# Performance work log

Hardware: AMD Instinct MI355X
Metric: run time of the kernel (lower is better)

## Reference

```python
import jax, jax.numpy as jnp
import numpy as np

B, N, E = 2, 50000, 400000
FIN, HID, OUT = 128, 128, 128
EPS = 1e-5  # BatchNorm1d default eps


def setup_inputs() -> dict:
    key = jax.random.key(0)
    ks = jax.random.split(key, 12)
    x = jax.random.normal(ks[0], (B, N, FIN), dtype=jnp.float32)
    row = jax.random.randint(ks[1], (E,), 0, N, dtype=jnp.int32)          # scatter dst
    col = jnp.concatenate([jnp.arange(N, dtype=jnp.int32),                # ensure deg>=1
                           jax.random.randint(ks[2], (E - N,), 0, N, dtype=jnp.int32)])
    edge_index = jnp.stack([row, col])                                    # [2, E]
    deg = jnp.zeros((N,), jnp.float32).at[col].add(1.0)                   # degree(col, N)
    dis = deg ** -0.5
    norm = (dis[row] * dis[col])[None, :, None]                           # [1, E, 1]
    W1 = jax.random.normal(ks[3], (HID, FIN), jnp.float32) / np.sqrt(FIN)
    b1 = jax.random.normal(ks[4], (HID,), jnp.float32) * 0.01
    g1 = jnp.ones((N,), jnp.float32)
    be1 = jnp.zeros((N,), jnp.float32)
    W2 = jax.random.normal(ks[5], (OUT, HID), jnp.float32) / np.sqrt(HID)
    b2 = jax.random.normal(ks[6], (OUT,), jnp.float32) * 0.01
    g2 = jnp.ones((N,), jnp.float32)
    be2 = jnp.zeros((N,), jnp.float32)
    return {"x": x, "edge_index": edge_index, "norm": norm,
            "W1": W1, "b1": b1, "g1": g1, "be1": be1,
            "W2": W2, "b2": b2, "g2": g2, "be2": be2}


def _gcn_layer(x, edge_index, norm, W, b, g, be):
    # Linear (dropout p=0 -> identity)
    h = jnp.einsum('bnf,of->bno', x, W) + b                 # [B, N, C]
    # BatchNorm1d(num_features=N): per-node stats over (batch, channel)
    mu = jnp.mean(h, axis=(0, 2), keepdims=True)            # [1, N, 1]
    var = jnp.var(h, axis=(0, 2), keepdims=True)            # biased, as torch
    y = g[None, :, None] * (h - mu) * jax.lax.rsqrt(var + EPS) + be[None, :, None]
    a = jax.nn.gelu(y, approximate=False)                   # torch GELU = exact erf
    # message passing: gather src nodes, scale by norm, scatter-add to dst
    msgs = a[:, edge_index[1], :] * norm                    # [B, E, C]
    return jnp.zeros_like(a).at[:, edge_index[0], :].add(msgs)


def reference(x, edge_index, norm, W1, b1, g1, be1, W2, b2, g2, be2):
    x = _gcn_layer(x, edge_index, norm, W1, b1, g1, be1)
    x = _gcn_layer(x, edge_index, norm, W2, b2, g2, be2)
    return x
```

## Files before the change

kernel.cpp:

```cpp
#include <hip/hip_runtime.h>
#include <math.h>

#define CC 128

typedef unsigned short u16;
typedef short bf16x8 __attribute__((ext_vector_type(8)));
typedef float f32x4 __attribute__((ext_vector_type(4)));

typedef __attribute__((address_space(3))) void lds_t;
typedef const __attribute__((address_space(1))) void gbl_t;

__device__ __forceinline__ u16 f2bf(float f) {
    union { float f; unsigned u; } v; v.f = f;
    unsigned u = v.u;
    return (u16)((u + 0x7FFFu + ((u >> 16) & 1u)) >> 16);
}
__device__ __forceinline__ float bf2f(unsigned hi16) {
    union { unsigned u; float f; } v; v.u = hi16 << 16; return v.f;
}
__device__ __forceinline__ unsigned cvt_pk(float lo, float hi) {
    unsigned r;
    asm("v_cvt_pk_bf16_f32 %0, %1, %2" : "=v"(r) : "v"(lo), "v"(hi));
    return r;
}

__device__ __forceinline__ float gelu_f(float y) {
    float xa = fabsf(y) * 0.70710678118654752f;
    float t  = __builtin_amdgcn_rcpf(fmaf(0.3275911f, xa, 1.0f));
    float p  = fmaf(1.061405429f, t, -1.453152027f);
    p = fmaf(p, t, 1.421413741f);
    p = fmaf(p, t, -0.284496736f);
    p = fmaf(p, t, 0.254829592f);
    p *= t;
    float e  = __expf(-xa * xa);
    float er = fmaf(-p, e, 1.0f);
    float s  = copysignf(er, y);
    return 0.5f * y * (1.0f + s);
}


__global__ __launch_bounds__(256) void k_zero_i32(int* __restrict__ p, int n) {
    int i = blockIdx.x * 256 + threadIdx.x;
    if (i < n) p[i] = 0;
}

__global__ __launch_bounds__(256) void k_hist(const int* __restrict__ row, int* __restrict__ cnt, int E) {
    int e = blockIdx.x * 256 + threadIdx.x;
    if (e < E) atomicAdd(&cnt[row[e]], 1);
}

__device__ __forceinline__ int wave_incl_scan(int v) {
    #pragma unroll
    for (int d = 1; d < 64; d <<= 1) {
        int t = __shfl_up(v, d);
        if ((threadIdx.x & 63) >= d) v += t;
    }
    return v;
}

__global__ __launch_bounds__(256) void k_scan_a(const int* __restrict__ cnt, int* __restrict__ bsum, int N) {
    int base = blockIdx.x * 1024 + threadIdx.x * 4;
    int s = 0;
    #pragma unroll
    for (int u = 0; u < 4; ++u) { int i = base + u; if (i < N) s += cnt[i]; }
    #pragma unroll
    for (int d = 32; d > 0; d >>= 1) s += __shfl_down(s, d);
    __shared__ int wsum[4];
    if ((threadIdx.x & 63) == 0) wsum[threadIdx.x >> 6] = s;
    __syncthreads();
    if (threadIdx.x == 0) bsum[blockIdx.x] = wsum[0] + wsum[1] + wsum[2] + wsum[3];
}

__global__ __launch_bounds__(64) void k_scan_b(const int* __restrict__ bsum, int* __restrict__ boff,
                                               int* __restrict__ off, int N, int nb) {
    int carry = 0;
    for (int base = 0; base < nb; base += 64) {
        int t = base + (int)threadIdx.x;
        int v = (t < nb) ? bsum[t] : 0;
        int incl = wave_incl_scan(v);
        if (t < nb) boff[t] = carry + incl - v;
        carry += __shfl(incl, 63);
    }
    if (threadIdx.x == 0) off[N] = carry;
}

__global__ __launch_bounds__(256) void k_scan_c(int* __restrict__ cnt, const int* __restrict__ boff,
                                                int* __restrict__ off, int N) {
    int t = threadIdx.x;
    int base = blockIdx.x * 1024 + t * 4;
    int v[4]; int s = 0;
    #pragma unroll
    for (int u = 0; u < 4; ++u) { int i = base + u; v[u] = (i < N) ? cnt[i] : 0; s += v[u]; }
    int incl = wave_incl_scan(s);
    __shared__ int wsum[4];
    int w = t >> 6, lane = t & 63;
    if (lane == 63) wsum[w] = incl;
    __syncthreads();
    int run = incl - s + boff[blockIdx.x];
    for (int ww = 0; ww < w; ++ww) run += wsum[ww];
    #pragma unroll
    for (int u = 0; u < 4; ++u) {
        int i = base + u;
        if (i < N) { off[i] = run; cnt[i] = 0; }
        run += v[u];
    }
}

__global__ __launch_bounds__(256) void k_fill(const int* __restrict__ row, const int* __restrict__ col,
                                              const float* __restrict__ nrm, const int* __restrict__ off,
                                              int* __restrict__ cur, int2* __restrict__ eg, int E) {
    int e = blockIdx.x * 256 + threadIdx.x;
    if (e < E) {
        int r = row[e];
        int p = off[r] + atomicAdd(&cur[r], 1);
        eg[p] = make_int2(col[e], __float_as_int(nrm[e]));
    }
}

__global__ __launch_bounds__(256) void k_wrepack(const float* __restrict__ W1, u16* __restrict__ Wp1,
                                                 const float* __restrict__ W2, u16* __restrict__ Wp2) {
    int i = blockIdx.x * 256 + threadIdx.x;
    if (i < 2 * CC * CC) {
        int is2 = (i >= CC * CC);
        int ii = is2 ? i - CC * CC : i;
        int j = ii & 7, l = (ii >> 3) & 63, s = (ii >> 9) & 3, t = ii >> 11;
        int r = 16 * t + (l & 15);
        int p = s * 32 + ((l >> 4) & 3) * 8 + j;
        if (is2) {
            int k = (p & 7) * 16 + (p >> 3);
            Wp2[ii] = f2bf(W2[r * CC + k]);
        } else {
            Wp1[ii] = f2bf(W1[r * CC + p]);
        }
    }
}

__global__ __launch_bounds__(256) void k_fused_l1(
    const float* __restrict__ X, const u16* __restrict__ Wp1, const u16* __restrict__ Wp2,
    const float* __restrict__ bias, const float* __restrict__ gamma, const float* __restrict__ beta,
    u16* __restrict__ Z, int N)
{
    __shared__ __align__(16) u16 WS[CC * CC];
    __shared__ __align__(16) unsigned TT[4][16][68];

    const int tid = threadIdx.x;
    const int w = tid >> 6;
    const int l = tid & 63;
    const int g = l >> 4;
    const int c = l & 15;
    const int n8 = blockIdx.x * 32 + w * 8;
    const bool valid = n8 < N;
    const int nbase = valid ? n8 : 0;

    #pragma unroll
    for (int it = 0; it < 8; ++it) {
        const u16* gsrc = Wp1 + it * 2048 + w * 512 + l * 8;
        u16* ldst = &WS[it * 2048 + w * 512];
        __builtin_amdgcn_global_load_lds((gbl_t*)gsrc, (lds_t*)ldst, 16, 0, 0);
    }

    const int ab = c >> 3;
    const int an = nbase + (c & 7);
    const float* xbase = X + ((size_t)ab * N + an) * CC + g * 8;
    bf16x8 af[4];
    #pragma unroll
    for (int s = 0; s < 4; ++s) {
        float4 lo = *(const float4*)(xbase + s * 32);
        float4 hi = *(const float4*)(xbase + s * 32 + 4);
        unsigned aw[4];
        aw[0] = cvt_pk(lo.x, lo.y); aw[1] = cvt_pk(lo.z, lo.w);
        aw[2] = cvt_pk(hi.x, hi.y); aw[3] = cvt_pk(hi.z, hi.w);
        af[s] = *(bf16x8*)aw;
    }

    float bb[8];
    #pragma unroll
    for (int t = 0; t < 8; ++t) bb[t] = bias[t * 16 + c];
    float gam[4], bet[4];
    #pragma unroll
    for (int r = 0; r < 4; ++r) {
        int p = (4 * g + r) & 7;
        gam[r] = gamma[nbase + p];
        bet[r] = beta[nbase + p];
    }

    __syncthreads();

    f32x4 acc[8];
    #pragma unroll
    for (int t = 0; t < 8; ++t) acc[t] = (f32x4){0.f, 0.f, 0.f, 0.f};
    #pragma unroll
    for (int s = 0; s < 4; ++s) {
        bf16x8 bf[8];
        #pragma unroll
        for (int t = 0; t < 8; ++t)
            bf[t] = *(const bf16x8*)&WS[((t * 4 + s) * 64 + l) * 8];
        #pragma unroll
        for (int t = 0; t < 8; ++t)
            acc[t] = __builtin_amdgcn_mfma_f32_16x16x32_bf16(af[s], bf[t], acc[t], 0, 0, 0);
    }

    __syncthreads();

    #pragma unroll
    for (int it = 0; it < 8; ++it) {
        const u16* gsrc = Wp2 + it * 2048 + w * 512 + l * 8;
        u16* ldst = &WS[it * 2048 + w * 512];
        __builtin_amdgcn_global_load_lds((gbl_t*)gsrc, (lds_t*)ldst, 16, 0, 0);
    }

    float rs[4] = {0.f, 0.f, 0.f, 0.f}, rq[4] = {0.f, 0.f, 0.f, 0.f};
    #pragma unroll
    for (int t = 0; t < 8; ++t)
        #pragma unroll
        for (int r = 0; r < 4; ++r) {
            float h = acc[t][r] + bb[t];
            acc[t][r] = h;
            rs[r] += h;
            rq[r] += h * h;
        }
    #pragma unroll
    for (int d = 1; d < 16; d <<= 1) {
        #pragma unroll
        for (int r = 0; r < 4; ++r) {
            rs[r] += __shfl_xor(rs[r], d);
            rq[r] += __shfl_xor(rq[r], d);
        }
    }
    #pragma unroll
    for (int r = 0; r < 4; ++r) {
        rs[r] += __shfl_xor(rs[r], 32);
        rq[r] += __shfl_xor(rq[r], 32);
    }

    #pragma unroll
    for (int r = 0; r < 4; ++r) {
        float mean = rs[r] * (1.f / 256.f);
        float var  = rq[r] * (1.f / 256.f) - mean * mean;
        float sc = gam[r] * rsqrtf(fmaxf(var, 0.f) + 1e-5f);
        float sh = bet[r] - mean * sc;
        #pragma unroll
        for (int t = 0; t < 8; ++t)
            acc[t][r] = gelu_f(acc[t][r] * sc + sh);
    }

    #pragma unroll
    for (int r = 0; r < 4; ++r) {
        unsigned tw[4];
        #pragma unroll
        for (int tt = 0; tt < 4; ++tt)
            tw[tt] = cvt_pk(acc[2 * tt][r], acc[2 * tt + 1][r]);
        *(uint4*)&TT[w][4 * g + r][c * 4] = *(uint4*)tw;
    }
    bf16x8 af2[4];
    #pragma unroll
    for (int s = 0; s < 4; ++s)
        af2[s] = *(const bf16x8*)&TT[w][c][s * 16 + g * 4];

    __syncthreads();

    f32x4 acc2[8];
    #pragma unroll
    for (int t = 0; t < 8; ++t) acc2[t] = (f32x4){0.f, 0.f, 0.f, 0.f};
    #pragma unroll
    for (int s = 0; s < 4; ++s) {
        bf16x8 bf[8];
        #pragma unroll
        for (int t = 0; t < 8; ++t)
            bf[t] = *(const bf16x8*)&WS[((t * 4 + s) * 64 + l) * 8];
        #pragma unroll
        for (int t = 0; t < 8; ++t)
            acc2[t] = __builtin_amdgcn_mfma_f32_16x16x32_bf16(af2[s], bf[t], acc2[t], 0, 0, 0);
    }

    if (valid) {
        #pragma unroll
        for (int r = 0; r < 4; ++r) {
            int rr = 4 * g + r;
            int db = rr >> 3, dn = n8 + (rr & 7);
            unsigned zw[4];
            #pragma unroll
            for (int tt = 0; tt < 4; ++tt)
                zw[tt] = cvt_pk(acc2[2 * tt][r], acc2[2 * tt + 1][r]);
            *(uint4*)(Z + ((size_t)dn * 2 + db) * CC + c * 8) = *(uint4*)zw;
        }
    }
}

__global__ __launch_bounds__(256) void k_agg_bn(
    const u16* __restrict__ Zin, const int* __restrict__ off, const int2* __restrict__ eg,
    const float* __restrict__ b2, const float* __restrict__ g2, const float* __restrict__ be2,
    u16* __restrict__ A2, int N)
{
    __shared__ u16 TW[4][256];
    int wv = threadIdx.x >> 6;
    int n = blockIdx.x * 4 + wv;
    if (n >= N) return;
    int l = threadIdx.x & 63;
    int p = l >> 5;
    int b = (l >> 4) & 1;
    int c = l & 15;
    const u16* Ab = Zin + b * CC + c * 8;
    int s = off[n], e = off[n + 1];
    float a[8] = {0.f, 0.f, 0.f, 0.f, 0.f, 0.f, 0.f, 0.f};
    for (int j = s; j < e; j += 8) {
        int i0 = j + p, i1 = j + 2 + p, i2 = j + 4 + p, i3 = j + 6 + p;
        int2 e0 = (i0 < e) ? eg[i0] : make_int2(0, 0);
        int2 e1 = (i1 < e) ? eg[i1] : make_int2(0, 0);
        int2 e2 = (i2 < e) ? eg[i2] : make_int2(0, 0);
        int2 e3 = (i3 < e) ? eg[i3] : make_int2(0, 0);
        bf16x8 v0 = *(const bf16x8*)(Ab + (size_t)e0.x * 256);
        bf16x8 v1 = *(const bf16x8*)(Ab + (size_t)e1.x * 256);
        bf16x8 v2 = *(const bf16x8*)(Ab + (size_t)e2.x * 256);
        bf16x8 v3 = *(const bf16x8*)(Ab + (size_t)e3.x * 256);
        float w0 = __int_as_float(e0.y), w1 = __int_as_float(e1.y);
        float w2 = __int_as_float(e2.y), w3 = __int_as_float(e3.y);
        #pragma unroll
        for (int q = 0; q < 8; ++q) {
            a[q] = fmaf(w0, bf2f((u16)v0[q]), a[q]);
            a[q] = fmaf(w1, bf2f((u16)v1[q]), a[q]);
            a[q] = fmaf(w2, bf2f((u16)v2[q]), a[q]);
            a[q] = fmaf(w3, bf2f((u16)v3[q]), a[q]);
        }
    }
    #pragma unroll
    for (int q = 0; q < 8; ++q) a[q] += __shfl_xor(a[q], 32);

    float ss = 0.f, qq = 0.f;
    #pragma unroll
    for (int t = 0; t < 8; ++t) {
        float h = a[t] + b2[t * 16 + c];
        a[t] = h;
        ss += h;
        qq += h * h;
    }
    #pragma unroll
    for (int d = 1; d < 32; d <<= 1) {
        ss += __shfl_xor(ss, d);
        qq += __shfl_xor(qq, d);
    }
    float mean = ss * (1.f / 256.f);
    float var  = qq * (1.f / 256.f) - mean * mean;
    float sc = g2[n] * rsqrtf(fmaxf(var, 0.f) + 1e-5f);
    float sh = be2[n] - mean * sc;

    if (l < 32) {
        #pragma unroll
        for (int t = 0; t < 8; ++t)
            TW[wv][b * CC + t * 16 + c] = f2bf(gelu_f(a[t] * sc + sh));
    }
    if (l < 32) {
        bf16x8 v = *(const bf16x8*)&TW[wv][l * 8];
        *(bf16x8*)(A2 + (size_t)n * 256 + l * 8) = v;
    }
}

__global__ __launch_bounds__(256) void k_agg_out(
    const u16* __restrict__ A2, const int* __restrict__ off, const int2* __restrict__ eg,
    float* __restrict__ Out, int N)
{
    int n = blockIdx.x * 4 + (threadIdx.x >> 6);
    if (n >= N) return;
    int l = threadIdx.x & 63;
    int p = l >> 5;
    int sl = l & 31;
    const u16* Ab = A2 + sl * 8;
    int s = off[n], e = off[n + 1];
    float a[8] = {0.f, 0.f, 0.f, 0.f, 0.f, 0.f, 0.f, 0.f};
    for (int j = s; j < e; j += 8) {
        int i0 = j + p, i1 = j + 2 + p, i2 = j + 4 + p, i3 = j + 6 + p;
        int2 e0 = (i0 < e) ? eg[i0] : make_int2(0, 0);
        int2 e1 = (i1 < e) ? eg[i1] : make_int2(0, 0);
        int2 e2 = (i2 < e) ? eg[i2] : make_int2(0, 0);
        int2 e3 = (i3 < e) ? eg[i3] : make_int2(0, 0);
        bf16x8 v0 = *(const bf16x8*)(Ab + (size_t)e0.x * 256);
        bf16x8 v1 = *(const bf16x8*)(Ab + (size_t)e1.x * 256);
        bf16x8 v2 = *(const bf16x8*)(Ab + (size_t)e2.x * 256);
        bf16x8 v3 = *(const bf16x8*)(Ab + (size_t)e3.x * 256);
        float w0 = __int_as_float(e0.y), w1 = __int_as_float(e1.y);
        float w2 = __int_as_float(e2.y), w3 = __int_as_float(e3.y);
        #pragma unroll
        for (int q = 0; q < 8; ++q) {
            a[q] = fmaf(w0, bf2f((u16)v0[q]), a[q]);
            a[q] = fmaf(w1, bf2f((u16)v1[q]), a[q]);
            a[q] = fmaf(w2, bf2f((u16)v2[q]), a[q]);
            a[q] = fmaf(w3, bf2f((u16)v3[q]), a[q]);
        }
    }
    #pragma unroll
    for (int q = 0; q < 8; ++q) a[q] += __shfl_xor(a[q], 32);
    if (l < 32) {
        int b = sl >> 4;
        int ch0 = (sl & 15) * 8;
        float* d = Out + ((size_t)b * N + n) * CC + ch0;
        *(float4*)&d[0] = make_float4(a[0], a[1], a[2], a[3]);
        *(float4*)&d[4] = make_float4(a[4], a[5], a[6], a[7]);
    }
}


extern "C" void kernel_launch(void* const* d_in, const int* in_sizes, int n_in,
                              void* d_out, int out_size, void* d_ws, size_t ws_size,
                              hipStream_t stream)
{
    const float* x   = (const float*)d_in[0];
    const int*   ei  = (const int*)d_in[1];
    const float* nrm = (const float*)d_in[2];
    const float* W1  = (const float*)d_in[3];
    const float* b1  = (const float*)d_in[4];
    const float* g1  = (const float*)d_in[5];
    const float* be1 = (const float*)d_in[6];
    const float* W2  = (const float*)d_in[7];
    const float* b2  = (const float*)d_in[8];
    const float* g2  = (const float*)d_in[9];
    const float* be2 = (const float*)d_in[10];

    const int N = in_sizes[5];
    const int E = in_sizes[2];
    const int* row = ei;
    const int* col = ei + E;
    const int nb = (N + 1023) / 1024;

    auto al = [](size_t v) { return (v + 255) & ~(size_t)255; };
    char* p = (char*)d_ws;
    int* off    = (int*)p;   p += al((size_t)(N + 1) * 4);
    int* cur    = (int*)p;   p += al((size_t)N * 4);
    int2* eg    = (int2*)p;  p += al((size_t)E * 8);
    int* bsum   = (int*)p;   p += al((size_t)nb * 4);
    int* boff   = (int*)p;   p += al((size_t)nb * 4);
    u16* Wp1    = (u16*)p;   p += al((size_t)CC * CC * 2);
    u16* Wp2    = (u16*)p;   p += al((size_t)CC * CC * 2);
    u16* Zbuf   = (u16*)p;   p += al((size_t)2 * N * CC * 2);
    u16* A2buf  = (u16*)p;   p += al((size_t)2 * N * CC * 2);

    k_zero_i32<<<(N + 255) / 256, 256, 0, stream>>>(cur, N);
    k_hist<<<(E + 255) / 256, 256, 0, stream>>>(row, cur, E);
    k_scan_a<<<nb, 256, 0, stream>>>(cur, bsum, N);
    k_scan_b<<<1, 64, 0, stream>>>(bsum, boff, off, N, nb);
    k_scan_c<<<nb, 256, 0, stream>>>(cur, boff, off, N);
    k_fill<<<(E + 255) / 256, 256, 0, stream>>>(row, col, nrm, off, cur, eg, E);

    k_wrepack<<<(2 * CC * CC + 255) / 256, 256, 0, stream>>>(W1, Wp1, W2, Wp2);

    const int gb = (N + 31) / 32;
    const int ga = (N + 3) / 4;
    k_fused_l1<<<gb, 256, 0, stream>>>(x, Wp1, Wp2, b1, g1, be1, Zbuf, N);
    k_agg_bn<<<ga, 256, 0, stream>>>(Zbuf, off, eg, b2, g2, be2, A2buf, N);
    k_agg_out<<<ga, 256, 0, stream>>>(A2buf, off, eg, (float*)d_out, N);
}
```

Before: 161.0 us.

## Use persistent grid-stride waves and vectorized edge loads in aggregation kernels

Both aggregation kernels now launch a fixed grid of 2048 blocks, and each wave loops over nodes in grid-stride fashion instead of one node per wave. The bias vector is hoisted out of the node loop. Edge records are read as two 16-byte loads of four contiguous edges per half-wave instead of four scalar int2 loads. The final writes are spread across all 64 lanes rather than 32. The edge buffer is padded so the vector loads can read past the end, which aims to cut block launch overhead and edge-load instruction count, at the cost of less dynamic load balancing across nodes.

```diff
diff --git a/kernel.cpp b/kernel.cpp
--- a/kernel.cpp
+++ b/kernel.cpp
@@ -290,111 +290,112 @@
 __global__ __launch_bounds__(256) void k_agg_bn(
     const u16* __restrict__ Zin, const int* __restrict__ off, const int2* __restrict__ eg,
     const float* __restrict__ b2, const float* __restrict__ g2, const float* __restrict__ be2,
-    u16* __restrict__ A2, int N)
+    u16* __restrict__ A2, int N, int nw)
 {
     __shared__ u16 TW[4][256];
-    int wv = threadIdx.x >> 6;
-    int n = blockIdx.x * 4 + wv;
-    if (n >= N) return;
-    int l = threadIdx.x & 63;
-    int p = l >> 5;
-    int b = (l >> 4) & 1;
-    int c = l & 15;
+    const int wv = threadIdx.x >> 6;
+    const int l = threadIdx.x & 63;
+    const int p = l >> 5;
+    const int b = (l >> 4) & 1;
+    const int c = l & 15;
     const u16* Ab = Zin + b * CC + c * 8;
-    int s = off[n], e = off[n + 1];
-    float a[8] = {0.f, 0.f, 0.f, 0.f, 0.f, 0.f, 0.f, 0.f};
-    for (int j = s; j < e; j += 8) {
-        int i0 = j + p, i1 = j + 2 + p, i2 = j + 4 + p, i3 = j + 6 + p;
-        int2 e0 = (i0 < e) ? eg[i0] : make_int2(0, 0);
-        int2 e1 = (i1 < e) ? eg[i1] : make_int2(0, 0);
-        int2 e2 = (i2 < e) ? eg[i2] : make_int2(0, 0);
-        int2 e3 = (i3 < e) ? eg[i3] : make_int2(0, 0);
-        bf16x8 v0 = *(const bf16x8*)(Ab + (size_t)e0.x * 256);
-        bf16x8 v1 = *(const bf16x8*)(Ab + (size_t)e1.x * 256);
-        bf16x8 v2 = *(const bf16x8*)(Ab + (size_t)e2.x * 256);
-        bf16x8 v3 = *(const bf16x8*)(Ab + (size_t)e3.x * 256);
-        float w0 = __int_as_float(e0.y), w1 = __int_as_float(e1.y);
-        float w2 = __int_as_float(e2.y), w3 = __int_as_float(e3.y);
-        #pragma unroll
-        for (int q = 0; q < 8; ++q) {
-            a[q] = fmaf(w0, bf2f((u16)v0[q]), a[q]);
-            a[q] = fmaf(w1, bf2f((u16)v1[q]), a[q]);
-            a[q] = fmaf(w2, bf2f((u16)v2[q]), a[q]);
-            a[q] = fmaf(w3, bf2f((u16)v3[q]), a[q]);
-        }
-    }
-    #pragma unroll
-    for (int q = 0; q < 8; ++q) a[q] += __shfl_xor(a[q], 32);
-
-    float ss = 0.f, qq = 0.f;
-    #pragma unroll
-    for (int t = 0; t < 8; ++t) {
-        float h = a[t] + b2[t * 16 + c];
-        a[t] = h;
-        ss += h;
-        qq += h * h;
-    }
-    #pragma unroll
-    for (int d = 1; d < 32; d <<= 1) {
-        ss += __shfl_xor(ss, d);
-        qq += __shfl_xor(qq, d);
-    }
-    float mean = ss * (1.f / 256.f);
-    float var  = qq * (1.f / 256.f) - mean * mean;
-    float sc = g2[n] * rsqrtf(fmaxf(var, 0.f) + 1e-5f);
-    float sh = be2[n] - mean * sc;
-
-    if (l < 32) {
-        #pragma unroll
-        for (int t = 0; t < 8; ++t)
-            TW[wv][b * CC + t * 16 + c] = f2bf(gelu_f(a[t] * sc + sh));
-    }
-    if (l < 32) {
-        bf16x8 v = *(const bf16x8*)&TW[wv][l * 8];
-        *(bf16x8*)(A2 + (size_t)n * 256 + l * 8) = v;
+    float bb[8];
+    #pragma unroll
+    for (int t = 0; t < 8; ++t) bb[t] = b2[t * 16 + c];
+
+    for (int n = blockIdx.x * 4 + wv; n < N; n += nw) {
+        int s = off[n], e = off[n + 1];
+        float a[8] = {0.f, 0.f, 0.f, 0.f, 0.f, 0.f, 0.f, 0.f};
+        for (int j = s; j < e; j += 8) {
+            int base = j + 4 * p;
+            uint4 ea = *(const uint4*)&eg[base];
+            uint4 eb = *(const uint4*)&eg[base + 2];
+            int s0 = (base     < e) ? (int)ea.x : 0; float w0 = (base     < e) ? __int_as_float((int)ea.y) : 0.f;
+            int s1 = (base + 1 < e) ? (int)ea.z : 0; float w1 = (base + 1 < e) ? __int_as_float((int)ea.w) : 0.f;
+            int s2 = (base + 2 < e) ? (int)eb.x : 0; float w2 = (base + 2 < e) ? __int_as_float((int)eb.y) : 0.f;
+            int s3 = (base + 3 < e) ? (int)eb.z : 0; float w3 = (base + 3 < e) ? __int_as_float((int)eb.w) : 0.f;
+            bf16x8 v0 = *(const bf16x8*)(Ab + (size_t)s0 * 256);
+            bf16x8 v1 = *(const bf16x8*)(Ab + (size_t)s1 * 256);
+            bf16x8 v2 = *(const bf16x8*)(Ab + (size_t)s2 * 256);
+            bf16x8 v3 = *(const bf16x8*)(Ab + (size_t)s3 * 256);
+            #pragma unroll
+            for (int q = 0; q < 8; ++q) {
+                a[q] = fmaf(w0, bf2f((u16)v0[q]), a[q]);
+                a[q] = fmaf(w1, bf2f((u16)v1[q]), a[q]);
+                a[q] = fmaf(w2, bf2f((u16)v2[q]), a[q]);
+                a[q] = fmaf(w3, bf2f((u16)v3[q]), a[q]);
+            }
+        }
+        #pragma unroll
+        for (int q = 0; q < 8; ++q) a[q] += __shfl_xor(a[q], 32);
+
+        float ss = 0.f, qq = 0.f;
+        #pragma unroll
+        for (int t = 0; t < 8; ++t) {
+            float h = a[t] + bb[t];
+            a[t] = h;
+            ss += h;
+            qq += h * h;
+        }
+        #pragma unroll
+        for (int d = 1; d < 32; d <<= 1) {
+            ss += __shfl_xor(ss, d);
+            qq += __shfl_xor(qq, d);
+        }
+        float mean = ss * (1.f / 256.f);
+        float var  = qq * (1.f / 256.f) - mean * mean;
+        float sc = g2[n] * rsqrtf(fmaxf(var, 0.f) + 1e-5f);
+        float sh = be2[n] - mean * sc;
+
+        #pragma unroll
+        for (int u = 0; u < 4; ++u) {
+            int q = 4 * p + u;
+            TW[wv][b * CC + q * 16 + c] = f2bf(gelu_f(a[q] * sc + sh));
+        }
+        uint2 v = *(const uint2*)&TW[wv][l * 4];
+        *(uint2*)(A2 + (size_t)n * 256 + l * 4) = v;
     }
 }
 
 __global__ __launch_bounds__(256) void k_agg_out(
     const u16* __restrict__ A2, const int* __restrict__ off, const int2* __restrict__ eg,
-    float* __restrict__ Out, int N)
+    float* __restrict__ Out, int N, int nw)
 {
-    int n = blockIdx.x * 4 + (threadIdx.x >> 6);
-    if (n >= N) return;
-    int l = threadIdx.x & 63;
-    int p = l >> 5;
-    int sl = l & 31;
+    const int l = threadIdx.x & 63;
+    const int p = l >> 5;
+    const int sl = l & 31;
     const u16* Ab = A2 + sl * 8;
-    int s = off[n], e = off[n + 1];
-    float a[8] = {0.f, 0.f, 0.f, 0.f, 0.f, 0.f, 0.f, 0.f};
-    for (int j = s; j < e; j += 8) {
-        int i0 = j + p, i1 = j + 2 + p, i2 = j + 4 + p, i3 = j + 6 + p;
-        int2 e0 = (i0 < e) ? eg[i0] : make_int2(0, 0);
-        int2 e1 = (i1 < e) ? eg[i1] : make_int2(0, 0);
-        int2 e2 = (i2 < e) ? eg[i2] : make_int2(0, 0);
-        int2 e3 = (i3 < e) ? eg[i3] : make_int2(0, 0);
-        bf16x8 v0 = *(const bf16x8*)(Ab + (size_t)e0.x * 256);
-        bf16x8 v1 = *(const bf16x8*)(Ab + (size_t)e1.x * 256);
-        bf16x8 v2 = *(const bf16x8*)(Ab + (size_t)e2.x * 256);
-        bf16x8 v3 = *(const bf16x8*)(Ab + (size_t)e3.x * 256);
-        float w0 = __int_as_float(e0.y), w1 = __int_as_float(e1.y);
-        float w2 = __int_as_float(e2.y), w3 = __int_as_float(e3.y);
-        #pragma unroll
-        for (int q = 0; q < 8; ++q) {
-            a[q] = fmaf(w0, bf2f((u16)v0[q]), a[q]);
-            a[q] = fmaf(w1, bf2f((u16)v1[q]), a[q]);
-            a[q] = fmaf(w2, bf2f((u16)v2[q]), a[q]);
-            a[q] = fmaf(w3, bf2f((u16)v3[q]), a[q]);
-        }
-    }
-    #pragma unroll
-    for (int q = 0; q < 8; ++q) a[q] += __shfl_xor(a[q], 32);
-    if (l < 32) {
-        int b = sl >> 4;
+
+    for (int n = blockIdx.x * 4 + (threadIdx.x >> 6); n < N; n += nw) {
+        int s = off[n], e = off[n + 1];
+        float a[8] = {0.f, 0.f, 0.f, 0.f, 0.f, 0.f, 0.f, 0.f};
+        for (int j = s; j < e; j += 8) {
+            int base = j + 4 * p;
+            uint4 ea = *(const uint4*)&eg[base];
+            uint4 eb = *(const uint4*)&eg[base + 2];
+            int s0 = (base     < e) ? (int)ea.x : 0; float w0 = (base     < e) ? __int_as_float((int)ea.y) : 0.f;
+            int s1 = (base + 1 < e) ? (int)ea.z : 0; float w1 = (base + 1 < e) ? __int_as_float((int)ea.w) : 0.f;
+            int s2 = (base + 2 < e) ? (int)eb.x : 0; float w2 = (base + 2 < e) ? __int_as_float((int)eb.y) : 0.f;
+            int s3 = (base + 3 < e) ? (int)eb.z : 0; float w3 = (base + 3 < e) ? __int_as_float((int)eb.w) : 0.f;
+            bf16x8 v0 = *(const bf16x8*)(Ab + (size_t)s0 * 256);
+            bf16x8 v1 = *(const bf16x8*)(Ab + (size_t)s1 * 256);
+            bf16x8 v2 = *(const bf16x8*)(Ab + (size_t)s2 * 256);
+            bf16x8 v3 = *(const bf16x8*)(Ab + (size_t)s3 * 256);
+            #pragma unroll
+            for (int q = 0; q < 8; ++q) {
+                a[q] = fmaf(w0, bf2f((u16)v0[q]), a[q]);
+                a[q] = fmaf(w1, bf2f((u16)v1[q]), a[q]);
+                a[q] = fmaf(w2, bf2f((u16)v2[q]), a[q]);
+                a[q] = fmaf(w3, bf2f((u16)v3[q]), a[q]);
+            }
+        }
+        #pragma unroll
+        for (int q = 0; q < 8; ++q) a[q] += __shfl_xor(a[q], 32);
+
+        int bb_ = sl >> 4;
         int ch0 = (sl & 15) * 8;
-        float* d = Out + ((size_t)b * N + n) * CC + ch0;
-        *(float4*)&d[0] = make_float4(a[0], a[1], a[2], a[3]);
-        *(float4*)&d[4] = make_float4(a[4], a[5], a[6], a[7]);
+        float* d = Out + ((size_t)bb_ * N + n) * CC + ch0 + 4 * p;
+        *(float4*)d = make_float4(a[4 * p + 0], a[4 * p + 1], a[4 * p + 2], a[4 * p + 3]);
     }
 }
 
@@ -425,7 +426,7 @@
     char* p = (char*)d_ws;
     int* off    = (int*)p;   p += al((size_t)(N + 1) * 4);
     int* cur    = (int*)p;   p += al((size_t)N * 4);
-    int2* eg    = (int2*)p;  p += al((size_t)E * 8);
+    int2* eg    = (int2*)p;  p += al((size_t)(E + 8) * 8);
     int* bsum   = (int*)p;   p += al((size_t)nb * 4);
     int* boff   = (int*)p;   p += al((size_t)nb * 4);
     u16* Wp1    = (u16*)p;   p += al((size_t)CC * CC * 2);
@@ -443,8 +444,9 @@
     k_wrepack<<<(2 * CC * CC + 255) / 256, 256, 0, stream>>>(W1, Wp1, W2, Wp2);
 
     const int gb = (N + 31) / 32;
-    const int ga = (N + 3) / 4;
+    const int AGG_BLOCKS = 2048;
+    const int nwaves = AGG_BLOCKS * 4;
     k_fused_l1<<<gb, 256, 0, stream>>>(x, Wp1, Wp2, b1, g1, be1, Zbuf, N);
-    k_agg_bn<<<ga, 256, 0, stream>>>(Zbuf, off, eg, b2, g2, be2, A2buf, N);
-    k_agg_out<<<ga, 256, 0, stream>>>(A2buf, off, eg, (float*)d_out, N);
-}
+    k_agg_bn<<<AGG_BLOCKS, 256, 0, stream>>>(Zbuf, off, eg, b2, g2, be2, A2buf, N, nwaves);
+    k_agg_out<<<AGG_BLOCKS, 256, 0, stream>>>(A2buf, off, eg, (float*)d_out, N, nwaves);
+}
```

Measured after the change: 165.6 us. 2.9% more time.
